# Kernel optimization log

Measured on AMD Instinct MI355X. Metric: run time of the kernel, lower is better.

The kernel has to match this reference:

```python
import math
import jax, jax.numpy as jnp
import numpy as np

LOG_NORM = -0.5 * math.log(2.0 * math.pi)  # per-dim gaussian normalizer
HEADS = 4
EM_ITERS = 5


def _mab(x, wq, bq, wk, bk, wv, bv, wo, bo):
    # Set-Transformer SAB(x) = MAB(x, x), ln=False
    B, S, D = x.shape
    dh = D // HEADS
    q = (x @ wq + bq).reshape(B, S, HEADS, dh)
    k = (x @ wk + bk).reshape(B, S, HEADS, dh)
    v = (x @ wv + bv).reshape(B, S, HEADS, dh)
    att = jax.nn.softmax(jnp.einsum('bqhd,bkhd->bhqk', q, k) / math.sqrt(D), axis=-1)
    o = q + jnp.einsum('bhqk,bkhd->bqhd', att, v)
    o = o.reshape(B, S, D)
    return o + jax.nn.relu(o @ wo + bo)


def setup_inputs() -> dict:
    key = jax.random.key(0)
    ks = jax.random.split(key, 16)
    B, S, D, L, K, MC = 16, 256, 512, 64, 20, 10
    s512 = 1.0 / math.sqrt(512.0)
    inp = {
        'H': jax.random.normal(ks[0], (B, S, D), jnp.float32),
        'eps': jax.random.normal(ks[1], (B * S, MC, L), jnp.float32),
        'sab_wq': jax.random.normal(ks[2], (2, D, D), jnp.float32) * s512,
        'sab_bq': jnp.zeros((2, D), jnp.float32),
        'sab_wk': jax.random.normal(ks[3], (2, D, D), jnp.float32) * s512,
        'sab_bk': jnp.zeros((2, D), jnp.float32),
        'sab_wv': jax.random.normal(ks[4], (2, D, D), jnp.float32) * s512,
        'sab_bv': jnp.zeros((2, D), jnp.float32),
        'sab_wo': jax.random.normal(ks[5], (2, D, D), jnp.float32) * s512,
        'sab_bo': jnp.zeros((2, D), jnp.float32),
        'wz': jax.random.normal(ks[6], (D, 2 * L), jnp.float32) * 0.02,
        'bz': jnp.zeros((2 * L,), jnp.float32),
        'w1': jax.random.normal(ks[7], (L, 2 * D), jnp.float32) * (1.0 / math.sqrt(L)),
        'b1': jnp.zeros((2 * D,), jnp.float32),
        'w2': jax.random.normal(ks[8], (2 * D, 2 * D), jnp.float32) * (1.0 / math.sqrt(2 * D)),
        'b2': jnp.zeros((2 * D,), jnp.float32),
        'w3': jax.random.normal(ks[9], (2 * D, D), jnp.float32) * (1.0 / math.sqrt(2 * D)),
        'b3': jnp.zeros((D,), jnp.float32),
    }
    rng = np.random.default_rng(1)
    # component_size distinct indices into the S*MC latent samples, per batch
    inp['init_idx'] = jnp.asarray(
        np.stack([rng.permutation(S * MC)[:K] for _ in range(B)]).astype(np.int32))
    return inp


def reference(H, eps, init_idx, sab_wq, sab_bq, sab_wk, sab_bk, sab_wv, sab_bv,
              sab_wo, sab_bo, wz, bz, w1, b1, w2, b2, w3, b3):
    B, S, D = H.shape
    MC, L = eps.shape[1], eps.shape[2]
    K = init_idx.shape[1]

    # q(z|x): two SABs + linear head
    h = H
    for i in range(2):
        h = _mab(h, sab_wq[i], sab_bq[i], sab_wk[i], sab_bk[i],
                 sab_wv[i], sab_bv[i], sab_wo[i], sab_bo[i])
    stats = h @ wz + bz                                    # [B,S,2L]
    mean, logvar = stats[..., :L], stats[..., L:]
    std = jnp.exp(0.5 * logvar)
    z = mean.reshape(B * S, 1, L) + eps * std.reshape(B * S, 1, L)
    z = z.reshape(B, S, MC, L)
    all_z = z.reshape(B, S * MC, L)                        # [B,N,L]

    # unsupervised EM prior (unit-variance GMM); distances via expansion
    pi = jnp.full((B, K), 1.0 / K, dtype=H.dtype)
    mu = jnp.take_along_axis(all_z, init_idx[:, :, None], axis=1)  # [B,K,L]
    x2 = jnp.sum(all_z * all_z, axis=-1)                   # [B,N]
    for _ in range(EM_ITERS):
        m2 = jnp.sum(mu * mu, axis=-1)                     # [B,K]
        ll = (-0.5 * (x2[:, :, None] - 2.0 * jnp.einsum('bnd,bkd->bnk', all_z, mu)
                      + m2[:, None, :]) + L * LOG_NORM + jnp.log(pi)[:, None, :])
        post = jax.nn.softmax(ll, axis=-1)                 # [B,N,K]
        Nk = post.sum(axis=1)                              # [B,K]
        pi = Nk / Nk.sum(axis=-1, keepdims=True)
        mu = jnp.einsum('bnk,bnd->bkd', post, all_z) / Nk[:, :, None]
    pi = jax.lax.stop_gradient(pi)
    mu = jax.lax.stop_gradient(mu)

    # reconstruction
    zf = z.reshape(-1, L)
    hr = jax.nn.relu(zf @ w1 + b1)
    hr = jax.nn.relu(hr @ w2 + b2)
    hr = jax.nn.relu(hr @ w3 + b3)
    hr = hr.reshape(B, S, MC, D)
    rec_loss = jnp.sum((hr - H[:, :, None, :]) ** 2) / (B * S * MC)

    # KL
    log_qz = jnp.sum(-0.5 * (logvar[:, :, None, :]
                             + (z - mean[:, :, None, :]) ** 2 / jnp.exp(logvar)[:, :, None, :])
                     + LOG_NORM, axis=-1)                  # [B,S,MC]
    z2 = jnp.sum(z * z, axis=-1)                           # [B,S,MC]
    m2 = jnp.sum(mu * mu, axis=-1)                         # [B,K]
    ll = (-0.5 * (z2[..., None] - 2.0 * jnp.einsum('bsmd,bkd->bsmk', z, mu)
                  + m2[:, None, None, :]) + L * LOG_NORM + jnp.log(pi)[:, None, None, :])
    log_pz = jax.scipy.special.logsumexp(ll, axis=-1)      # [B,S,MC]
    kl_loss = jnp.mean(log_qz - log_pz)
    return rec_loss, kl_loss
```

## Files before the change

### kernel.cpp

```cpp
#include <hip/hip_runtime.h>
#include <hip/hip_bf16.h>
#include <math.h>


#define BATCH 16
#define SEQ 256
#define DIM 512
#define NH 4
#define DH 128
#define LD 64
#define KC 20
#define MC 10
#define NPTS 2560
#define BS_TOT 4096
#define NROWS 40960
#define LOG_NORM (-0.9189385332046727f)

typedef __attribute__((ext_vector_type(8))) short bf16x8;
typedef __attribute__((ext_vector_type(4))) float f32x4;
typedef __hip_bfloat16 bf;

__device__ inline float warpReduceSum(float v) {
    for (int o = 32; o > 0; o >>= 1) v += __shfl_down(v, o);
    return v;
}
__device__ inline float warpReduceMax(float v) {
    for (int o = 32; o > 0; o >>= 1) v = fmaxf(v, __shfl_down(v, o));
    return v;
}

__device__ inline void async_copy16(const bf* g, bf* l) {
    __builtin_amdgcn_global_load_lds(
        (const __attribute__((address_space(1))) unsigned int*)g,
        (__attribute__((address_space(3))) unsigned int*)l, 16, 0, 0);
}

__device__ inline void split_store(float x, bf* ph, bf* pl, long idx) {
    const bf h = __float2bfloat16(x);
    ph[idx] = h;
    pl[idx] = __float2bfloat16(x - __bfloat162float(h));
}

template<int MODE>
__global__ __launch_bounds__(256, 3)
void gemm3t(const bf* __restrict__ Ah, const bf* __restrict__ Al,
            const bf* __restrict__ Bh, const bf* __restrict__ Bl,
            int K, int lda, int ldb,
            const float* __restrict__ b0, const float* __restrict__ b1v,
            const float* __restrict__ b2v,
            float* __restrict__ outF,
            bf* __restrict__ P1h, bf* __restrict__ P1l,
            bf* __restrict__ P2h, bf* __restrict__ P2l,
            bf* __restrict__ P3h, bf* __restrict__ P3l,
            const bf* __restrict__ Rh, const bf* __restrict__ Rl)
{
    __shared__ __align__(16) char smem[24576];
    bf* Ash = (bf*)smem;
    bf* Asl = (bf*)(smem + 4096);
    bf* Bsh = (bf*)(smem + 8192);
    bf* Bsl = (bf*)(smem + 16384);
    float* Xs = (float*)smem;

    const int t = threadIdx.x;
    const int m0 = blockIdx.y * 64, n0 = blockIdx.x * 128;
    const int w = t >> 6, lane = t & 63;
    const int wn = w * 32;
    const int fm = lane & 15, quad = lane >> 4, fk = quad * 8;
    const int srow = t >> 2, scol = (t & 3) * 8;

    f32x4 acc[4][2];
#pragma unroll
    for (int i = 0; i < 4; i++)
#pragma unroll
        for (int j = 0; j < 2; j++) acc[i][j] = (f32x4){0.f, 0.f, 0.f, 0.f};

    const int nk = K >> 5;
    for (int kk = 0; kk < nk; kk++) {
        const long ao = (long)(m0 + srow) * lda + kk * 32 + scol;
        const long bo = (long)(n0 + srow) * ldb + kk * 32 + scol;
        async_copy16(Ah + ao, Ash + w * 512);
        async_copy16(Al + ao, Asl + w * 512);
        async_copy16(Bh + bo, Bsh + w * 512);
        async_copy16(Bh + bo + 64L * ldb, Bsh + 2048 + w * 512);
        async_copy16(Bl + bo, Bsl + w * 512);
        async_copy16(Bl + bo + 64L * ldb, Bsl + 2048 + w * 512);
        __syncthreads();

        bf16x8 afh[4], afl[4], bfh[2], bfl[2];
#pragma unroll
        for (int mi = 0; mi < 4; mi++) {
            afh[mi] = *(const bf16x8*)&Ash[(mi * 16 + fm) * 32 + fk];
            afl[mi] = *(const bf16x8*)&Asl[(mi * 16 + fm) * 32 + fk];
        }
#pragma unroll
        for (int ni = 0; ni < 2; ni++) {
            bfh[ni] = *(const bf16x8*)&Bsh[(wn + ni * 16 + fm) * 32 + fk];
            bfl[ni] = *(const bf16x8*)&Bsl[(wn + ni * 16 + fm) * 32 + fk];
        }
#pragma unroll
        for (int mi = 0; mi < 4; mi++)
#pragma unroll
            for (int ni = 0; ni < 2; ni++) {
                acc[mi][ni] = __builtin_amdgcn_mfma_f32_16x16x32_bf16(
                    afh[mi], bfh[ni], acc[mi][ni], 0, 0, 0);
                acc[mi][ni] = __builtin_amdgcn_mfma_f32_16x16x32_bf16(
                    afh[mi], bfl[ni], acc[mi][ni], 0, 0, 0);
                acc[mi][ni] = __builtin_amdgcn_mfma_f32_16x16x32_bf16(
                    afl[mi], bfh[ni], acc[mi][ni], 0, 0, 0);
            }
        __syncthreads();
    }

    const int rl = t >> 2;
    const int cc4 = (t & 3) * 16;

    for (int p = 0; p < 2; p++) {
        if ((w >> 1) == p) {
            const int cb = wn - p * 64;
#pragma unroll
            for (int mi = 0; mi < 4; mi++)
#pragma unroll
                for (int ni = 0; ni < 2; ni++) {
                    const int c = cb + ni * 16 + fm;
#pragma unroll
                    for (int r = 0; r < 4; r++)
                        Xs[(mi * 16 + quad * 4 + r) * 68 + c] = acc[mi][ni][r];
                }
        }
        __syncthreads();

        if (MODE == 0 && n0 >= 1024) {
            const int hh = (n0 >> 7) & 3;
            const int dd = p * 64 + rl;
            const int bb = m0 >> 8;
            const int sb = (m0 & 255) + cc4;
            const float bias = b2v[hh * 128 + dd];
            const long ob = (((long)(bb * NH + hh) * DH + dd) << 8) + sb;
#pragma unroll
            for (int j = 0; j < 2; j++) {
                bf16x8 vh, vl;
#pragma unroll
                for (int i = 0; i < 8; i++) {
                    const float x = Xs[(cc4 + j * 8 + i) * 68 + rl] + bias;
                    const bf h = __float2bfloat16(x);
                    vh[i] = *(const short*)&h;
                    const bf l = __float2bfloat16(x - __bfloat162float(h));
                    vl[i] = *(const short*)&l;
                }
                *(bf16x8*)&P3h[ob + j * 8] = vh;
                *(bf16x8*)&P3l[ob + j * 8] = vl;
            }
        } else {
            float xv[16];
#pragma unroll
            for (int i = 0; i < 4; i++)
                *(float4*)&xv[i * 4] = *(const float4*)&Xs[rl * 68 + cc4 + i * 4];

            if (MODE == 0) {
                const int which = n0 >> 9;
                const int colq = (n0 & 511) + p * 64 + cc4;
                const float* bias = which ? b1v : b0;
                bf* Ph = which ? P2h : P1h;
                bf* Pl = which ? P2l : P1l;
                const long ob = (long)(m0 + rl) * 512 + colq;
#pragma unroll
                for (int j = 0; j < 2; j++) {
                    bf16x8 vh, vl;
#pragma unroll
                    for (int i = 0; i < 8; i++) {
                        const float x = xv[j * 8 + i] + bias[colq + j * 8 + i];
                        const bf h = __float2bfloat16(x); vh[i] = *(const short*)&h;
                        const bf l = __float2bfloat16(x - __bfloat162float(h));
                        vl[i] = *(const short*)&l;
                    }
                    *(bf16x8*)&Ph[ob + j * 8] = vh;
                    *(bf16x8*)&Pl[ob + j * 8] = vl;
                }
            } else if (MODE == 3) {
                const int colg = n0 + p * 64 + cc4;
                const long ob = (long)(m0 + rl) * 512 + colg;
#pragma unroll
                for (int j = 0; j < 2; j++) {
                    const bf16x8 rh = *(const bf16x8*)&Rh[ob + j * 8];
                    const bf16x8 rv = *(const bf16x8*)&Rl[ob + j * 8];
                    bf16x8 vh, vl;
#pragma unroll
                    for (int i = 0; i < 8; i++) {
                        short sh = rh[i], sl = rv[i];
                        float x = fmaxf(xv[j * 8 + i] + b0[colg + j * 8 + i], 0.f)
                                + __bfloat162float(*(const bf*)&sh)
                                + __bfloat162float(*(const bf*)&sl);
                        const bf h = __float2bfloat16(x); vh[i] = *(const short*)&h;
                        const bf l = __float2bfloat16(x - __bfloat162float(h));
                        vl[i] = *(const short*)&l;
                    }
                    *(bf16x8*)&P1h[ob + j * 8] = vh;
                    *(bf16x8*)&P1l[ob + j * 8] = vl;
                }
            } else {
                const int colg = p * 64 + cc4;
                const long ob = (long)(m0 + rl) * 128 + colg;
#pragma unroll
                for (int i = 0; i < 4; i++) {
                    float4 v = *(float4*)&xv[i * 4];
                    v.x += b0[colg + i * 4 + 0];
                    v.y += b0[colg + i * 4 + 1];
                    v.z += b0[colg + i * 4 + 2];
                    v.w += b0[colg + i * 4 + 3];
                    *(float4*)&outF[ob + i * 4] = v;
                }
            }
        }
        __syncthreads();
    }
}

__global__ __launch_bounds__(256)
void attn_fused(const bf* __restrict__ qh, const bf* __restrict__ ql,
                const bf* __restrict__ kh, const bf* __restrict__ kl,
                const bf* __restrict__ vTh, const bf* __restrict__ vTl,
                bf* __restrict__ oh, bf* __restrict__ ol)
{
    __shared__ __align__(16) char smem[43008];
    bf* Qsh = (bf*)smem;            bf* Qsl = (bf*)(smem + 4096);
    bf* Ksh = (bf*)(smem + 8192);   bf* Ksl = (bf*)(smem + 24576);
    bf* Psh = (bf*)smem;            bf* Psl = (bf*)(smem + 4096);
    bf* Vsh = (bf*)(smem + 8192);   bf* Vsl = (bf*)(smem + 16384);
    float (*red)[4]  = (float(*)[4])(smem + 40960);
    float (*red2)[4] = (float(*)[4])(smem + 41984);

    const int t = threadIdx.x;
    const int z = blockIdx.y;
    const int m0 = blockIdx.x * 64;
    const int bb = z >> 2, hh = z & 3;
    const long hOff = (long)bb * 131072 + (long)hh * 128;
    const long vOff = (long)z * 32768;

    const int w = t >> 6, lane = t & 63;
    const int fm = lane & 15;
    const int quad = lane >> 4;
    const int fk = quad * 8;
    const int srow = t >> 2, scol = (t & 3) * 8;

    f32x4 acc[4][4];
#pragma unroll
    for (int i = 0; i < 4; i++)
#pragma unroll
        for (int j = 0; j < 4; j++) acc[i][j] = (f32x4){0.f, 0.f, 0.f, 0.f};

    for (int kk = 0; kk < 4; kk++) {
        const long ao = hOff + (long)(m0 + srow) * 512 + kk * 32 + scol;
        const long bo = hOff + (long)srow * 512 + kk * 32 + scol;
        async_copy16(qh + ao, Qsh + w * 512);
        async_copy16(ql + ao, Qsl + w * 512);
#pragma unroll
        for (int j = 0; j < 4; j++) {
            async_copy16(kh + bo + (long)j * 64 * 512, Ksh + w * 512 + j * 2048);
            async_copy16(kl + bo + (long)j * 64 * 512, Ksl + w * 512 + j * 2048);
        }
        __syncthreads();

        bf16x8 afh[4], afl[4];
#pragma unroll
        for (int mi = 0; mi < 4; mi++) {
            afh[mi] = *(const bf16x8*)&Qsh[(mi * 16 + fm) * 32 + fk];
            afl[mi] = *(const bf16x8*)&Qsl[(mi * 16 + fm) * 32 + fk];
        }
#pragma unroll
        for (int ni = 0; ni < 4; ni++) {
            const bf16x8 bh = *(const bf16x8*)&Ksh[(w * 64 + ni * 16 + fm) * 32 + fk];
            const bf16x8 bl = *(const bf16x8*)&Ksl[(w * 64 + ni * 16 + fm) * 32 + fk];
#pragma unroll
            for (int mi = 0; mi < 4; mi++) {
                acc[mi][ni] = __builtin_amdgcn_mfma_f32_16x16x32_bf16(
                    afh[mi], bh, acc[mi][ni], 0, 0, 0);
                acc[mi][ni] = __builtin_amdgcn_mfma_f32_16x16x32_bf16(
                    afh[mi], bl, acc[mi][ni], 0, 0, 0);
                acc[mi][ni] = __builtin_amdgcn_mfma_f32_16x16x32_bf16(
                    afl[mi], bh, acc[mi][ni], 0, 0, 0);
            }
        }
        __syncthreads();
    }

    const float alpha = 0.044194173824159216f;
#pragma unroll
    for (int mi = 0; mi < 4; mi++)
#pragma unroll
        for (int r = 0; r < 4; r++) {
            float m = -1e30f;
#pragma unroll
            for (int ni = 0; ni < 4; ni++) m = fmaxf(m, acc[mi][ni][r]);
            for (int o = 8; o > 0; o >>= 1) m = fmaxf(m, __shfl_xor(m, o));
            if (fm == 0) red[mi * 16 + quad * 4 + r][w] = m;
        }
    __syncthreads();
    float invr[4][4];
#pragma unroll
    for (int mi = 0; mi < 4; mi++)
#pragma unroll
        for (int r = 0; r < 4; r++) {
            const int rowl = mi * 16 + quad * 4 + r;
            const float mx = fmaxf(fmaxf(red[rowl][0], red[rowl][1]),
                                   fmaxf(red[rowl][2], red[rowl][3]));
            float s = 0.f;
#pragma unroll
            for (int ni = 0; ni < 4; ni++) {
                const float e = __expf((acc[mi][ni][r] - mx) * alpha);
                acc[mi][ni][r] = e;
                s += e;
            }
            for (int o = 8; o > 0; o >>= 1) s += __shfl_xor(s, o);
            if (fm == 0) red2[rowl][w] = s;
        }
    __syncthreads();
#pragma unroll
    for (int mi = 0; mi < 4; mi++)
#pragma unroll
        for (int r = 0; r < 4; r++) {
            const int rowl = mi * 16 + quad * 4 + r;
            invr[mi][r] = 1.f / (red2[rowl][0] + red2[rowl][1] + red2[rowl][2] + red2[rowl][3]);
        }

    f32x4 acc2[4][2];
#pragma unroll
    for (int i = 0; i < 4; i++)
#pragma unroll
        for (int j = 0; j < 2; j++) acc2[i][j] = (f32x4){0.f, 0.f, 0.f, 0.f};

    for (int kc = 0; kc < 8; kc++) {
        if (w == (kc >> 1)) {
            const int nib = (kc & 1) * 2;
#pragma unroll
            for (int mi = 0; mi < 4; mi++)
#pragma unroll
                for (int r = 0; r < 4; r++) {
                    const int row = mi * 16 + quad * 4 + r;
#pragma unroll
                    for (int j = 0; j < 2; j++) {
                        const float p = acc[mi][nib + j][r] * invr[mi][r];
                        const int cc = j * 16 + fm;
                        const bf h = __float2bfloat16(p);
                        Psh[row * 32 + cc] = h;
                        Psl[row * 32 + cc] = __float2bfloat16(p - __bfloat162float(h));
                    }
                }
        }
        const long vo = vOff + (long)srow * 256 + kc * 32 + scol;
        async_copy16(vTh + vo, Vsh + w * 512);
        async_copy16(vTh + vo + 64L * 256, Vsh + w * 512 + 2048);
        async_copy16(vTl + vo, Vsl + w * 512);
        async_copy16(vTl + vo + 64L * 256, Vsl + w * 512 + 2048);
        __syncthreads();

        bf16x8 pfh[4], pfl[4];
#pragma unroll
        for (int mi = 0; mi < 4; mi++) {
            pfh[mi] = *(const bf16x8*)&Psh[(mi * 16 + fm) * 32 + fk];
            pfl[mi] = *(const bf16x8*)&Psl[(mi * 16 + fm) * 32 + fk];
        }
#pragma unroll
        for (int ni = 0; ni < 2; ni++) {
            const bf16x8 vh = *(const bf16x8*)&Vsh[(w * 32 + ni * 16 + fm) * 32 + fk];
            const bf16x8 vl = *(const bf16x8*)&Vsl[(w * 32 + ni * 16 + fm) * 32 + fk];
#pragma unroll
            for (int mi = 0; mi < 4; mi++) {
                acc2[mi][ni] = __builtin_amdgcn_mfma_f32_16x16x32_bf16(
                    pfh[mi], vh, acc2[mi][ni], 0, 0, 0);
                acc2[mi][ni] = __builtin_amdgcn_mfma_f32_16x16x32_bf16(
                    pfh[mi], vl, acc2[mi][ni], 0, 0, 0);
                acc2[mi][ni] = __builtin_amdgcn_mfma_f32_16x16x32_bf16(
                    pfl[mi], vh, acc2[mi][ni], 0, 0, 0);
            }
        }
        __syncthreads();
    }

#pragma unroll
    for (int ni = 0; ni < 2; ni++) {
        const int col = hh * 128 + w * 32 + ni * 16 + fm;
#pragma unroll
        for (int mi = 0; mi < 4; mi++)
#pragma unroll
            for (int r = 0; r < 4; r++) {
                const int row = mi * 16 + quad * 4 + r;
                const long idx = (long)(bb * 256 + m0 + row) * 512 + col;
                const float x = acc2[mi][ni][r]
                    + __bfloat162float(qh[idx]) + __bfloat162float(ql[idx]);
                split_store(x, oh, ol, idx);
            }
    }
}

template<bool SQLOSS>
__global__ __launch_bounds__(256, 3)
void gemm_mfma(const bf* __restrict__ A, const bf* __restrict__ BT,
               bf* __restrict__ C,
               const float* __restrict__ bias,
               const float* __restrict__ Href,
               float* __restrict__ lossAcc,
               int K, int N)
{
    __shared__ __align__(16) char smem[17408];
    bf* Asg = (bf*)smem;
    bf* Bsg = (bf*)(smem + 8192);
    bf* Cs  = (bf*)smem;
    __shared__ float redS[4];

    const int t = threadIdx.x;
    const int flat = blockIdx.y * gridDim.x + blockIdx.x;
    const int lane8 = flat & 7;
    const int grp = flat >> 3;
    const int n_blk = grp % gridDim.x;
    const int m_blk = (grp / gridDim.x) * 8 + lane8;
    const int m0 = m_blk * 128, n0 = n_blk * 128;

    const int w = t >> 6, lane = t & 63;
    const int wm = (w >> 1) * 64, wn = (w & 1) * 64;
    const int fm = lane & 15;
    const int quad = lane >> 4;
    const int fk = quad * 8;
    const int srow = t >> 2, scol = (t & 3) * 8;

    f32x4 acc[4][4];
#pragma unroll
    for (int i = 0; i < 4; i++)
#pragma unroll
        for (int j = 0; j < 4; j++) acc[i][j] = (f32x4){0.f, 0.f, 0.f, 0.f};

    const int nk = K >> 5;
    for (int kt = 0; kt < nk; kt++) {
        const bf* ga = A + (long)(m0 + srow) * K + kt * 32 + scol;
        const bf* gb = BT + (long)(n0 + srow) * K + kt * 32 + scol;
        async_copy16(ga, Asg + w * 512);
        async_copy16(ga + 64L * K, Asg + 2048 + w * 512);
        async_copy16(gb, Bsg + w * 512);
        async_copy16(gb + 64L * K, Bsg + 2048 + w * 512);
        __syncthreads();

        bf16x8 af[4], bfr[4];
#pragma unroll
        for (int mi = 0; mi < 4; mi++)
            af[mi] = *(const bf16x8*)&Asg[(wm + mi * 16 + fm) * 32 + fk];
#pragma unroll
        for (int ni = 0; ni < 4; ni++)
            bfr[ni] = *(const bf16x8*)&Bsg[(wn + ni * 16 + fm) * 32 + fk];
#pragma unroll
        for (int mi = 0; mi < 4; mi++)
#pragma unroll
            for (int ni = 0; ni < 4; ni++)
                acc[mi][ni] = __builtin_amdgcn_mfma_f32_16x16x32_bf16(
                    af[mi], bfr[ni], acc[mi][ni], 0, 0, 0);
        __syncthreads();
    }

    if (SQLOSS) {
        float lsum = 0.f;
#pragma unroll
        for (int ni = 0; ni < 4; ni++) {
            const int col = n0 + wn + ni * 16 + fm;
            const float b = bias[col];
#pragma unroll
            for (int mi = 0; mi < 4; mi++)
#pragma unroll
                for (int r = 0; r < 4; r++) {
                    const int row = m0 + wm + mi * 16 + quad * 4 + r;
                    const float x = fmaxf(acc[mi][ni][r] + b, 0.f);
                    const float d = x - Href[(long)(row / MC) * DIM + col];
                    lsum = fmaf(d, d, lsum);
                }
        }
        lsum = warpReduceSum(lsum);
        if (lane == 0) redS[w] = lsum;
        __syncthreads();
        if (t == 0) atomicAdd(lossAcc, redS[0] + redS[1] + redS[2] + redS[3]);
    } else {
        for (int hf = 0; hf < 2; hf++) {
            if ((w >> 1) == hf) {
#pragma unroll
                for (int ni = 0; ni < 4; ni++) {
                    const int c = wn + ni * 16 + fm;
                    const float bv = bias[n0 + c];
#pragma unroll
                    for (int mi = 0; mi < 4; mi++)
#pragma unroll
                        for (int r = 0; r < 4; r++) {
                            const float x = fmaxf(acc[mi][ni][r] + bv, 0.f);
                            Cs[(mi * 16 + quad * 4 + r) * 136 + c] = __float2bfloat16(x);
                        }
                }
            }
            __syncthreads();
            const int rl2 = t >> 2, cc2 = (t & 3) * 32;
            const long ob = (long)(m0 + hf * 64 + rl2) * N + n0 + cc2;
#pragma unroll
            for (int j = 0; j < 4; j++)
                *(bf16x8*)&C[ob + j * 8] = *(const bf16x8*)&Cs[rl2 * 136 + cc2 + j * 8];
            __syncthreads();
        }
    }
}

__global__ void conv_all_weights(
    const float* __restrict__ wq, const float* __restrict__ wk,
    const float* __restrict__ wv, const float* __restrict__ wo,
    bf* __restrict__ qkvTh0, bf* __restrict__ qkvTl0,
    bf* __restrict__ woTh0, bf* __restrict__ woTl0,
    bf* __restrict__ qkvTh1, bf* __restrict__ qkvTl1,
    bf* __restrict__ woTh1, bf* __restrict__ woTl1,
    const float* __restrict__ wz, bf* __restrict__ wzTh, bf* __restrict__ wzTl,
    const float* __restrict__ w1, bf* __restrict__ w1T,
    const float* __restrict__ w2, bf* __restrict__ w2T,
    const float* __restrict__ w3, bf* __restrict__ w3T)
{
    const int idx = blockIdx.x * 256 + threadIdx.x;
    if (idx < 2097152) {
        const int layer = idx >> 20;
        const int seg = (idx >> 18) & 3;
        const int r = idx & 262143;
        const int k = r >> 9, n = r & 511;
        const float* src = ((seg == 0) ? wq : (seg == 1) ? wk : (seg == 2) ? wv : wo)
                           + (long)layer * 262144;
        const float x = src[r];
        const bf h = __float2bfloat16(x);
        const bf l = __float2bfloat16(x - __bfloat162float(h));
        if (seg < 3) {
            const long o = (long)(seg * 512 + n) * 512 + k;
            if (layer == 0) { qkvTh0[o] = h; qkvTl0[o] = l; }
            else            { qkvTh1[o] = h; qkvTl1[o] = l; }
        } else {
            const long o = (long)n * 512 + k;
            if (layer == 0) { woTh0[o] = h; woTl0[o] = l; }
            else            { woTh1[o] = h; woTl1[o] = l; }
        }
    } else if (idx < 2162688) {
        const int i = idx - 2097152;
        const int k = i >> 7, n = i & 127;
        const float x = wz[i];
        const bf h = __float2bfloat16(x);
        wzTh[(long)n * 512 + k] = h;
        wzTl[(long)n * 512 + k] = __float2bfloat16(x - __bfloat162float(h));
    } else if (idx < 2228224) {
        const int i = idx - 2162688;
        const int k = i >> 10, n = i & 1023;
        w1T[(long)n * 64 + k] = __float2bfloat16(w1[i]);
    } else if (idx < 3276800) {
        const int i = idx - 2228224;
        const int k = i >> 10, n = i & 1023;
        w2T[(long)n * 1024 + k] = __float2bfloat16(w2[i]);
    } else if (idx < 3801088) {
        const int i = idx - 3276800;
        const int k = i >> 9, n = i & 511;
        w3T[(long)n * 1024 + k] = __float2bfloat16(w3[i]);
    }
}

__global__ void conv_split_flat(const float* __restrict__ src,
                                bf* __restrict__ dh, bf* __restrict__ dl, int n)
{
    const int i = blockIdx.x * 256 + threadIdx.x;
    if (i < n) {
        const float x = src[i];
        const bf h = __float2bfloat16(x);
        dh[i] = h;
        dl[i] = __float2bfloat16(x - __bfloat162float(h));
    }
}

__global__ __launch_bounds__(256)
void zgen(const float* __restrict__ stats, const float* __restrict__ eps,
          float* __restrict__ z, bf* __restrict__ z16)
{
    const int idx = blockIdx.x * 256 + threadIdx.x;
    const int bs = idx / 160;
    const int r = idx % 160;
    const int l4 = r % 16;
    const float4 e = ((const float4*)eps)[idx];
    const float4 mn = ((const float4*)stats)[bs * 32 + l4];
    const float4 lv = ((const float4*)stats)[bs * 32 + 16 + l4];
    float4 zz;
    zz.x = fmaf(e.x, expf(0.5f * lv.x), mn.x);
    zz.y = fmaf(e.y, expf(0.5f * lv.y), mn.y);
    zz.z = fmaf(e.z, expf(0.5f * lv.z), mn.z);
    zz.w = fmaf(e.w, expf(0.5f * lv.w), mn.w);
    ((float4*)z)[idx] = zz;
    bf* zp = z16 + (long)idx * 4;
    zp[0] = __float2bfloat16(zz.x);
    zp[1] = __float2bfloat16(zz.y);
    zp[2] = __float2bfloat16(zz.z);
    zp[3] = __float2bfloat16(zz.w);
}

__global__ void em_init(const float* __restrict__ z, const int* __restrict__ init_idx,
                        float* __restrict__ mu, float* __restrict__ logPi,
                        float* __restrict__ musum, float* __restrict__ NkG)
{
    const int b = blockIdx.x, t = threadIdx.x;
    for (int i = t; i < KC * LD; i += 256) {
        const int k = i >> 6, l = i & 63;
        const int idx = init_idx[b * KC + k];
        mu[b * KC * LD + i] = z[((long)b * NPTS + idx) * LD + l];
        musum[b * KC * LD + i] = 0.f;
    }
    if (t < KC) {
        logPi[b * KC + t] = -logf((float)KC);
        NkG[b * KC + t] = 0.f;
    }
}

__global__ __launch_bounds__(256)
void em_step(const float* __restrict__ z, const float* __restrict__ mu,
             const float* __restrict__ logPi,
             float* __restrict__ musum, float* __restrict__ NkG)
{
    __shared__ float muS[KC][65];
    __shared__ float m2lp[KC];
    __shared__ float postS[KC][256];
    __shared__ float NkS[KC];

    const int tile = blockIdx.x, b = blockIdx.y, t = threadIdx.x;

    for (int i = t; i < KC * LD; i += 256) muS[i >> 6][i & 63] = mu[b * KC * LD + i];
    __syncthreads();
    if (t < KC) {
        float s = 0.f;
        for (int l = 0; l < LD; l++) { const float m = muS[t][l]; s = fmaf(m, m, s); }
        m2lp[t] = -0.5f * s + logPi[b * KC + t];
    }
    __syncthreads();

    const long n = (long)tile * 256 + t;
    const float* zr = &z[((long)b * NPTS + n) * LD];
    float acc[KC];
#pragma unroll
    for (int k = 0; k < KC; k++) acc[k] = 0.f;
#pragma unroll
    for (int l4 = 0; l4 < 16; l4++) {
        const float4 zv = ((const float4*)zr)[l4];
#pragma unroll
        for (int k = 0; k < KC; k++) {
            acc[k] = fmaf(zv.x, muS[k][l4 * 4 + 0], acc[k]);
            acc[k] = fmaf(zv.y, muS[k][l4 * 4 + 1], acc[k]);
            acc[k] = fmaf(zv.z, muS[k][l4 * 4 + 2], acc[k]);
            acc[k] = fmaf(zv.w, muS[k][l4 * 4 + 3], acc[k]);
        }
    }
    float mx = -1e30f;
    float llv[KC];
#pragma unroll
    for (int k = 0; k < KC; k++) { llv[k] = acc[k] + m2lp[k]; mx = fmaxf(mx, llv[k]); }
    float s = 0.f;
#pragma unroll
    for (int k = 0; k < KC; k++) { llv[k] = expf(llv[k] - mx); s += llv[k]; }
    const float inv = 1.f / s;
#pragma unroll
    for (int k = 0; k < KC; k++) postS[k][t] = llv[k] * inv;
    __syncthreads();

    const int lane = t & 63, w = t >> 6;
#pragma unroll
    for (int kk = 0; kk < 5; kk++) {
        const int k = w * 5 + kk;
        float p = postS[k][lane] + postS[k][lane + 64] + postS[k][lane + 128] + postS[k][lane + 192];
        p = warpReduceSum(p);
        if (lane == 0) NkS[k] = p;
    }
    __syncthreads();

    const float* zb = &z[((long)b * NPTS + (long)tile * 256) * LD];
#pragma unroll
    for (int j = 0; j < 5; j++) {
        const int o = t + j * 256;
        const int k = o >> 6, l = o & 63;
        float sacc = 0.f;
        for (int n2 = 0; n2 < 256; n2++)
            sacc = fmaf(postS[k][n2], zb[n2 * LD + l], sacc);
        atomicAdd(&musum[b * KC * LD + o], sacc);
    }
    if (t < KC) atomicAdd(&NkG[b * KC + t], NkS[t]);
}

__global__ void em_update(float* __restrict__ mu, float* __restrict__ logPi,
                          float* __restrict__ musum, float* __restrict__ NkG)
{
    __shared__ float Nk[KC];
    const int b = blockIdx.x, t = threadIdx.x;
    if (t < KC) Nk[t] = NkG[b * KC + t];
    __syncthreads();
    float s = 0.f;
    for (int k = 0; k < KC; k++) s += Nk[k];
    if (t < KC) logPi[b * KC + t] = logf(Nk[t] / s);
    for (int i = t; i < KC * LD; i += 64) {
        const int k = i >> 6;
        mu[b * KC * LD + i] = musum[b * KC * LD + i] / Nk[k];
        musum[b * KC * LD + i] = 0.f;
    }
    __syncthreads();
    if (t < KC) NkG[b * KC + t] = 0.f;
}

__global__ __launch_bounds__(256)
void kl_kernel(const float* __restrict__ z, const float* __restrict__ stats,
               const float* __restrict__ eps,
               const float* __restrict__ mu, const float* __restrict__ logPi,
               float* __restrict__ klAcc)
{
    __shared__ float muS[KC][65];
    __shared__ float m2lp[KC];
    __shared__ float redS[4];

    const int tile = blockIdx.x, b = blockIdx.y, t = threadIdx.x;

    for (int i = t; i < KC * LD; i += 256) muS[i >> 6][i & 63] = mu[b * KC * LD + i];
    __syncthreads();
    if (t < KC) {
        float s = 0.f;
        for (int l = 0; l < LD; l++) { const float m = muS[t][l]; s = fmaf(m, m, s); }
        m2lp[t] = -0.5f * s + logPi[b * KC + t];
    }
    __syncthreads();

    const int n = tile * 256 + t;
    const int sidx = n / MC, m = n % MC;
    const long bs = (long)b * SEQ + sidx;
    const float* zr = &z[((long)b * NPTS + n) * LD];

    float acc[KC];
#pragma unroll
    for (int k = 0; k < KC; k++) acc[k] = 0.f;
    float x2 = 0.f;
#pragma unroll
    for (int l4 = 0; l4 < 16; l4++) {
        const float4 zv = ((const float4*)zr)[l4];
        x2 = fmaf(zv.x, zv.x, fmaf(zv.y, zv.y, fmaf(zv.z, zv.z, fmaf(zv.w, zv.w, x2))));
#pragma unroll
        for (int k = 0; k < KC; k++) {
            acc[k] = fmaf(zv.x, muS[k][l4 * 4 + 0], acc[k]);
            acc[k] = fmaf(zv.y, muS[k][l4 * 4 + 1], acc[k]);
            acc[k] = fmaf(zv.z, muS[k][l4 * 4 + 2], acc[k]);
            acc[k] = fmaf(zv.w, muS[k][l4 * 4 + 3], acc[k]);
        }
    }
    float mx = -1e30f;
    float llv[KC];
#pragma unroll
    for (int k = 0; k < KC; k++) { llv[k] = acc[k] + m2lp[k]; mx = fmaxf(mx, llv[k]); }
    float s = 0.f;
#pragma unroll
    for (int k = 0; k < KC; k++) s += expf(llv[k] - mx);
    const float log_pz = -0.5f * x2 + mx + logf(s) + LD * LOG_NORM;

    const float* lvr = &stats[bs * 128 + 64];
    const float* er = &eps[(bs * MC + m) * LD];
    float slv = 0.f, se2 = 0.f;
#pragma unroll
    for (int l4 = 0; l4 < 16; l4++) {
        const float4 lv = ((const float4*)lvr)[l4];
        slv += lv.x + lv.y + lv.z + lv.w;
        const float4 e = ((const float4*)er)[l4];
        se2 = fmaf(e.x, e.x, fmaf(e.y, e.y, fmaf(e.z, e.z, fmaf(e.w, e.w, se2))));
    }
    const float log_qz = -0.5f * (slv + se2) + LD * LOG_NORM;

    float v = log_qz - log_pz;
    v = warpReduceSum(v);
    if ((t & 63) == 0) redS[t >> 6] = v;
    __syncthreads();
    if (t == 0) atomicAdd(klAcc, redS[0] + redS[1] + redS[2] + redS[3]);
}

__global__ void finalize(const float* __restrict__ scal, float* __restrict__ out)
{
    if (threadIdx.x == 0) {
        out[0] = scal[0] * (1.f / (float)NROWS);
        out[1] = scal[1] * (1.f / (float)NROWS);
    }
}

extern "C" void kernel_launch(void* const* d_in, const int* in_sizes, int n_in,
                              void* d_out, int out_size, void* d_ws, size_t ws_size,
                              hipStream_t stream)
{
    const float* H   = (const float*)d_in[0];
    const float* eps = (const float*)d_in[1];
    const float* wq  = (const float*)d_in[2];
    const float* bq  = (const float*)d_in[3];
    const float* wk  = (const float*)d_in[4];
    const float* bk  = (const float*)d_in[5];
    const float* wv  = (const float*)d_in[6];
    const float* bv  = (const float*)d_in[7];
    const float* wo  = (const float*)d_in[8];
    const float* bo  = (const float*)d_in[9];
    const float* wz  = (const float*)d_in[10];
    const float* bz  = (const float*)d_in[11];
    const float* w1  = (const float*)d_in[12];
    const float* b1  = (const float*)d_in[13];
    const float* w2  = (const float*)d_in[14];
    const float* b2  = (const float*)d_in[15];
    const float* w3  = (const float*)d_in[16];
    const float* b3  = (const float*)d_in[17];
    const int* init_idx = (const int*)d_in[18];
    float* out = (float*)d_out;
    float* wsf = (float*)d_ws;

    const long o_scal  = 0;
    const long o_NkG   = 1024;
    const long o_musum = 2048;
    const long o_logpi = 23552;
    const long o_mu    = 24576;
    const long o_q     = 45056;
    const long o_k     = 2142208;
    const long o_vT    = 4239360;
    const long o_o     = 6336512;
    const long o_h1    = 8433664;
    const long o_qkvT0 = 10530816;
    const long o_woT0  = 11317248;
    const long o_qkvT1 = 11579392;
    const long o_woT1  = 12365824;
    const long o_wzT   = 12627968;
    const long o_st    = 12693504;
    const long o_zb    = 13217792;
    const long o_z16   = 15839232;
    const long o_w1T   = 17149952;
    const long o_w2T   = 17182720;
    const long o_w3T   = 17707008;
    const long o_d1    = 17969152;
    const long o_d2    = 38940672;

    const long PL = (long)BS_TOT * DIM;
    bf* qh  = (bf*)(wsf + o_q);   bf* ql  = qh + PL;
    bf* kh  = (bf*)(wsf + o_k);   bf* kl_ = kh + PL;
    bf* vTh = (bf*)(wsf + o_vT);  bf* vTl = vTh + PL;
    bf* oh  = (bf*)(wsf + o_o);   bf* ol  = oh + PL;
    bf* h1h = (bf*)(wsf + o_h1);  bf* h1l = h1h + PL;
    bf* h2h = qh;                 bf* h2l = ql;
    bf* qkvTh0 = (bf*)(wsf + o_qkvT0); bf* qkvTl0 = qkvTh0 + 1536L * 512;
    bf* woTh0  = (bf*)(wsf + o_woT0);  bf* woTl0  = woTh0 + 512L * 512;
    bf* qkvTh1 = (bf*)(wsf + o_qkvT1); bf* qkvTl1 = qkvTh1 + 1536L * 512;
    bf* woTh1  = (bf*)(wsf + o_woT1);  bf* woTl1  = woTh1 + 512L * 512;
    bf* wzTh = (bf*)(wsf + o_wzT);     bf* wzTl = wzTh + 128L * 512;
    bf* w1T = (bf*)(wsf + o_w1T);
    bf* w2T = (bf*)(wsf + o_w2T);
    bf* w3T = (bf*)(wsf + o_w3T);
    bf* z16 = (bf*)(wsf + o_z16);
    bf* d1  = (bf*)(wsf + o_d1);
    bf* d2  = (bf*)(wsf + o_d2);
    float* st = wsf + o_st;
    float* zb = wsf + o_zb;
    float* scal = wsf + o_scal;

    hipMemsetAsync(scal, 0, 64, stream);

    const dim3 blk(256);

    conv_split_flat<<<(int)((PL + 255) / 256), blk, 0, stream>>>(H, h1h, h1l, (int)PL);
    conv_all_weights<<<14848, blk, 0, stream>>>(
        wq, wk, wv, wo,
        qkvTh0, qkvTl0, woTh0, woTl0,
        qkvTh1, qkvTl1, woTh1, woTl1,
        wz, wzTh, wzTl, w1, w1T, w2, w2T, w3, w3T);

    for (int i = 0; i < 2; i++) {
        const long boff = (long)i * DIM;
        bf* qkh = i ? qkvTh1 : qkvTh0;  bf* qkl = i ? qkvTl1 : qkvTl0;
        bf* wh  = i ? woTh1 : woTh0;    bf* wl  = i ? woTl1 : woTl0;

        gemm3t<0><<<dim3(12, 64), blk, 0, stream>>>(
            h1h, h1l, qkh, qkl, 512, 512, 512,
            bq + boff, bk + boff, bv + boff, nullptr,
            qh, ql, kh, kl_, vTh, vTl, nullptr, nullptr);
        attn_fused<<<dim3(4, 64), blk, 0, stream>>>(qh, ql, kh, kl_, vTh, vTl, oh, ol);
        bf* houth = (i == 0) ? h1h : h2h;
        bf* houtl = (i == 0) ? h1l : h2l;
        gemm3t<3><<<dim3(4, 64), blk, 0, stream>>>(
            oh, ol, wh, wl, 512, 512, 512,
            bo + boff, nullptr, nullptr, nullptr,
            houth, houtl, nullptr, nullptr, nullptr, nullptr, oh, ol);
    }

    gemm3t<4><<<dim3(1, 64), blk, 0, stream>>>(
        h2h, h2l, wzTh, wzTl, 512, 512, 512,
        bz, nullptr, nullptr, st,
        nullptr, nullptr, nullptr, nullptr, nullptr, nullptr, nullptr, nullptr);

    zgen<<<2560, blk, 0, stream>>>(st, eps, zb, z16);

    gemm_mfma<false><<<dim3(8, 320), blk, 0, stream>>>(
        z16, w1T, d1, b1, nullptr, nullptr, 64, 1024);
    gemm_mfma<false><<<dim3(8, 320), blk, 0, stream>>>(
        d1, w2T, d2, b2, nullptr, nullptr, 1024, 1024);
    gemm_mfma<true><<<dim3(4, 320), blk, 0, stream>>>(
        d2, w3T, nullptr, b3, H, scal + 0, 1024, 512);

    em_init<<<16, blk, 0, stream>>>(zb, init_idx, wsf + o_mu, wsf + o_logpi,
                                    wsf + o_musum, wsf + o_NkG);
    for (int it = 0; it < 5; it++) {
        em_step<<<dim3(10, 16), blk, 0, stream>>>(zb, wsf + o_mu, wsf + o_logpi,
                                                  wsf + o_musum, wsf + o_NkG);
        em_update<<<16, 64, 0, stream>>>(wsf + o_mu, wsf + o_logpi,
                                         wsf + o_musum, wsf + o_NkG);
    }

    kl_kernel<<<dim3(10, 16), blk, 0, stream>>>(zb, st, eps, wsf + o_mu,
                                                wsf + o_logpi, scal + 1);

    finalize<<<1, 64, 0, stream>>>(scal, out);
}
```

Baseline: 713.8 us.

## Fuse z generation, EM loop and KL into one cooperative kernel

Replaces zgen, em_init, five em_step/em_update pairs and kl_kernel with a single cooperative kernel of 160 blocks that uses grid-wide syncs between phases. The H split conversion and the scalar zeroing move into the weight-conversion kernel, which removes the memset and one launch. This targets per-launch overhead and gaps across about 13 small dependent launches. In exchange it adds grid.sync costs, relies on all 160 blocks being co-resident, and zgen now runs on only 160 blocks instead of 2560.

Result: slower. 1.453 ms (+103.6%).

```diff
diff --git a/kernel.cpp b/kernel.cpp
--- a/kernel.cpp
+++ b/kernel.cpp
@@ -1,6 +1,9 @@
 #include <hip/hip_runtime.h>
 #include <hip/hip_bf16.h>
+#include <hip/hip_cooperative_groups.h>
 #include <math.h>
+
+namespace cg = cooperative_groups;
 
 
 #define BATCH 16
@@ -22,10 +25,6 @@
 
 __device__ inline float warpReduceSum(float v) {
     for (int o = 32; o > 0; o >>= 1) v += __shfl_down(v, o);
-    return v;
-}
-__device__ inline float warpReduceMax(float v) {
-    for (int o = 32; o > 0; o >>= 1) v = fmaxf(v, __shfl_down(v, o));
     return v;
 }
 
@@ -501,7 +500,8 @@
     }
 }
 
-__global__ void conv_all_weights(
+__global__ void conv_all(
+    const float* __restrict__ H, bf* __restrict__ h0h, bf* __restrict__ h0l,
     const float* __restrict__ wq, const float* __restrict__ wk,
     const float* __restrict__ wv, const float* __restrict__ wo,
     bf* __restrict__ qkvTh0, bf* __restrict__ qkvTl0,
@@ -511,9 +511,20 @@
     const float* __restrict__ wz, bf* __restrict__ wzTh, bf* __restrict__ wzTl,
     const float* __restrict__ w1, bf* __restrict__ w1T,
     const float* __restrict__ w2, bf* __restrict__ w2T,
-    const float* __restrict__ w3, bf* __restrict__ w3T)
+    const float* __restrict__ w3, bf* __restrict__ w3T,
+    float* __restrict__ scal)
 {
-    const int idx = blockIdx.x * 256 + threadIdx.x;
+    const int t = threadIdx.x;
+    if (blockIdx.x == 0 && t < 16) scal[t] = 0.f;
+    const int gidx = blockIdx.x * 256 + t;
+    if (gidx < 2097152) {
+        const float x = H[gidx];
+        const bf h = __float2bfloat16(x);
+        h0h[gidx] = h;
+        h0l[gidx] = __float2bfloat16(x - __bfloat162float(h));
+        return;
+    }
+    const int idx = gidx - 2097152;
     if (idx < 2097152) {
         const int layer = idx >> 20;
         const int seg = (idx >> 18) & 3;
@@ -555,70 +566,138 @@
     }
 }
 
-__global__ void conv_split_flat(const float* __restrict__ src,
-                                bf* __restrict__ dh, bf* __restrict__ dl, int n)
-{
-    const int i = blockIdx.x * 256 + threadIdx.x;
-    if (i < n) {
-        const float x = src[i];
-        const bf h = __float2bfloat16(x);
-        dh[i] = h;
-        dl[i] = __float2bfloat16(x - __bfloat162float(h));
-    }
-}
-
 __global__ __launch_bounds__(256)
-void zgen(const float* __restrict__ stats, const float* __restrict__ eps,
-          float* __restrict__ z, bf* __restrict__ z16)
-{
-    const int idx = blockIdx.x * 256 + threadIdx.x;
-    const int bs = idx / 160;
-    const int r = idx % 160;
-    const int l4 = r % 16;
-    const float4 e = ((const float4*)eps)[idx];
-    const float4 mn = ((const float4*)stats)[bs * 32 + l4];
-    const float4 lv = ((const float4*)stats)[bs * 32 + 16 + l4];
-    float4 zz;
-    zz.x = fmaf(e.x, expf(0.5f * lv.x), mn.x);
-    zz.y = fmaf(e.y, expf(0.5f * lv.y), mn.y);
-    zz.z = fmaf(e.z, expf(0.5f * lv.z), mn.z);
-    zz.w = fmaf(e.w, expf(0.5f * lv.w), mn.w);
-    ((float4*)z)[idx] = zz;
-    bf* zp = z16 + (long)idx * 4;
-    zp[0] = __float2bfloat16(zz.x);
-    zp[1] = __float2bfloat16(zz.y);
-    zp[2] = __float2bfloat16(zz.z);
-    zp[3] = __float2bfloat16(zz.w);
-}
-
-__global__ void em_init(const float* __restrict__ z, const int* __restrict__ init_idx,
-                        float* __restrict__ mu, float* __restrict__ logPi,
-                        float* __restrict__ musum, float* __restrict__ NkG)
-{
-    const int b = blockIdx.x, t = threadIdx.x;
-    for (int i = t; i < KC * LD; i += 256) {
-        const int k = i >> 6, l = i & 63;
-        const int idx = init_idx[b * KC + k];
-        mu[b * KC * LD + i] = z[((long)b * NPTS + idx) * LD + l];
-        musum[b * KC * LD + i] = 0.f;
-    }
-    if (t < KC) {
-        logPi[b * KC + t] = -logf((float)KC);
-        NkG[b * KC + t] = 0.f;
-    }
-}
-
-__global__ __launch_bounds__(256)
-void em_step(const float* __restrict__ z, const float* __restrict__ mu,
-             const float* __restrict__ logPi,
-             float* __restrict__ musum, float* __restrict__ NkG)
+void em_all(const float* __restrict__ stats, const float* __restrict__ eps,
+            const int* __restrict__ init_idx,
+            float* __restrict__ z, bf* __restrict__ z16,
+            float* __restrict__ mu, float* __restrict__ logPi,
+            float* __restrict__ musum, float* __restrict__ NkG,
+            float* __restrict__ klAcc)
 {
     __shared__ float muS[KC][65];
     __shared__ float m2lp[KC];
     __shared__ float postS[KC][256];
     __shared__ float NkS[KC];
-
-    const int tile = blockIdx.x, b = blockIdx.y, t = threadIdx.x;
+    __shared__ float NkU[KC];
+    __shared__ float redS[4];
+
+    cg::grid_group grid = cg::this_grid();
+    const int bx = blockIdx.x;
+    const int tile = bx % 10, b = bx / 10;
+    const int t = threadIdx.x;
+    const int lane = t & 63, w = t >> 6;
+
+    for (int i = 0; i < 16; i++) {
+        const int idx = bx * 4096 + i * 256 + t;
+        const int bs = idx / 160;
+        const int r = idx % 160;
+        const int l4 = r % 16;
+        const float4 e = ((const float4*)eps)[idx];
+        const float4 mn = ((const float4*)stats)[bs * 32 + l4];
+        const float4 lv = ((const float4*)stats)[bs * 32 + 16 + l4];
+        float4 zz;
+        zz.x = fmaf(e.x, expf(0.5f * lv.x), mn.x);
+        zz.y = fmaf(e.y, expf(0.5f * lv.y), mn.y);
+        zz.z = fmaf(e.z, expf(0.5f * lv.z), mn.z);
+        zz.w = fmaf(e.w, expf(0.5f * lv.w), mn.w);
+        ((float4*)z)[idx] = zz;
+        bf* zp = z16 + (long)idx * 4;
+        zp[0] = __float2bfloat16(zz.x);
+        zp[1] = __float2bfloat16(zz.y);
+        zp[2] = __float2bfloat16(zz.z);
+        zp[3] = __float2bfloat16(zz.w);
+    }
+    grid.sync();
+
+    if (tile == 0) {
+        for (int i = t; i < KC * LD; i += 256) {
+            const int k = i >> 6, l = i & 63;
+            const int idx = init_idx[b * KC + k];
+            mu[b * KC * LD + i] = z[((long)b * NPTS + idx) * LD + l];
+            musum[b * KC * LD + i] = 0.f;
+        }
+        if (t < KC) {
+            logPi[b * KC + t] = -logf((float)KC);
+            NkG[b * KC + t] = 0.f;
+        }
+    }
+    grid.sync();
+
+    for (int it = 0; it < 5; it++) {
+        for (int i = t; i < KC * LD; i += 256) muS[i >> 6][i & 63] = mu[b * KC * LD + i];
+        __syncthreads();
+        if (t < KC) {
+            float s = 0.f;
+            for (int l = 0; l < LD; l++) { const float m = muS[t][l]; s = fmaf(m, m, s); }
+            m2lp[t] = -0.5f * s + logPi[b * KC + t];
+        }
+        __syncthreads();
+
+        const long n = (long)tile * 256 + t;
+        const float* zr = &z[((long)b * NPTS + n) * LD];
+        float acc[KC];
+#pragma unroll
+        for (int k = 0; k < KC; k++) acc[k] = 0.f;
+#pragma unroll
+        for (int l4 = 0; l4 < 16; l4++) {
+            const float4 zv = ((const float4*)zr)[l4];
+#pragma unroll
+            for (int k = 0; k < KC; k++) {
+                acc[k] = fmaf(zv.x, muS[k][l4 * 4 + 0], acc[k]);
+                acc[k] = fmaf(zv.y, muS[k][l4 * 4 + 1], acc[k]);
+                acc[k] = fmaf(zv.z, muS[k][l4 * 4 + 2], acc[k]);
+                acc[k] = fmaf(zv.w, muS[k][l4 * 4 + 3], acc[k]);
+            }
+        }
+        float mx = -1e30f;
+        float llv[KC];
+#pragma unroll
+        for (int k = 0; k < KC; k++) { llv[k] = acc[k] + m2lp[k]; mx = fmaxf(mx, llv[k]); }
+        float s = 0.f;
+#pragma unroll
+        for (int k = 0; k < KC; k++) { llv[k] = expf(llv[k] - mx); s += llv[k]; }
+        const float inv = 1.f / s;
+#pragma unroll
+        for (int k = 0; k < KC; k++) postS[k][t] = llv[k] * inv;
+        __syncthreads();
+
+#pragma unroll
+        for (int kk = 0; kk < 5; kk++) {
+            const int k = w * 5 + kk;
+            float p = postS[k][lane] + postS[k][lane + 64] + postS[k][lane + 128] + postS[k][lane + 192];
+            p = warpReduceSum(p);
+            if (lane == 0) NkS[k] = p;
+        }
+        __syncthreads();
+
+        const float* zb = &z[((long)b * NPTS + (long)tile * 256) * LD];
+#pragma unroll
+        for (int j = 0; j < 5; j++) {
+            const int o = t + j * 256;
+            const int k = o >> 6, l = o & 63;
+            float sacc = 0.f;
+            for (int n2 = 0; n2 < 256; n2++)
+                sacc = fmaf(postS[k][n2], zb[n2 * LD + l], sacc);
+            atomicAdd(&musum[b * KC * LD + o], sacc);
+        }
+        if (t < KC) atomicAdd(&NkG[b * KC + t], NkS[t]);
+        grid.sync();
+
+        if (tile == 0) {
+            if (t < KC) NkU[t] = NkG[b * KC + t];
+            __syncthreads();
+            float sn = 0.f;
+            for (int k = 0; k < KC; k++) sn += NkU[k];
+            if (t < KC) logPi[b * KC + t] = logf(NkU[t] / sn);
+            for (int i = t; i < KC * LD; i += 256) {
+                mu[b * KC * LD + i] = musum[b * KC * LD + i] / NkU[i >> 6];
+                musum[b * KC * LD + i] = 0.f;
+            }
+            __syncthreads();
+            if (t < KC) NkG[b * KC + t] = 0.f;
+        }
+        grid.sync();
+    }
 
     for (int i = t; i < KC * LD; i += 256) muS[i >> 6][i & 63] = mu[b * KC * LD + i];
     __syncthreads();
@@ -629,144 +708,55 @@
     }
     __syncthreads();
 
-    const long n = (long)tile * 256 + t;
-    const float* zr = &z[((long)b * NPTS + n) * LD];
-    float acc[KC];
-#pragma unroll
-    for (int k = 0; k < KC; k++) acc[k] = 0.f;
-#pragma unroll
-    for (int l4 = 0; l4 < 16; l4++) {
-        const float4 zv = ((const float4*)zr)[l4];
-#pragma unroll
-        for (int k = 0; k < KC; k++) {
-            acc[k] = fmaf(zv.x, muS[k][l4 * 4 + 0], acc[k]);
-            acc[k] = fmaf(zv.y, muS[k][l4 * 4 + 1], acc[k]);
-            acc[k] = fmaf(zv.z, muS[k][l4 * 4 + 2], acc[k]);
-            acc[k] = fmaf(zv.w, muS[k][l4 * 4 + 3], acc[k]);
-        }
-    }
-    float mx = -1e30f;
-    float llv[KC];
-#pragma unroll
-    for (int k = 0; k < KC; k++) { llv[k] = acc[k] + m2lp[k]; mx = fmaxf(mx, llv[k]); }
-    float s = 0.f;
-#pragma unroll
-    for (int k = 0; k < KC; k++) { llv[k] = expf(llv[k] - mx); s += llv[k]; }
-    const float inv = 1.f / s;
-#pragma unroll
-    for (int k = 0; k < KC; k++) postS[k][t] = llv[k] * inv;
-    __syncthreads();
-
-    const int lane = t & 63, w = t >> 6;
-#pragma unroll
-    for (int kk = 0; kk < 5; kk++) {
-        const int k = w * 5 + kk;
-        float p = postS[k][lane] + postS[k][lane + 64] + postS[k][lane + 128] + postS[k][lane + 192];
-        p = warpReduceSum(p);
-        if (lane == 0) NkS[k] = p;
-    }
-    __syncthreads();
-
-    const float* zb = &z[((long)b * NPTS + (long)tile * 256) * LD];
-#pragma unroll
-    for (int j = 0; j < 5; j++) {
-        const int o = t + j * 256;
-        const int k = o >> 6, l = o & 63;
-        float sacc = 0.f;
-        for (int n2 = 0; n2 < 256; n2++)
-            sacc = fmaf(postS[k][n2], zb[n2 * LD + l], sacc);
-        atomicAdd(&musum[b * KC * LD + o], sacc);
-    }
-    if (t < KC) atomicAdd(&NkG[b * KC + t], NkS[t]);
-}
-
-__global__ void em_update(float* __restrict__ mu, float* __restrict__ logPi,
-                          float* __restrict__ musum, float* __restrict__ NkG)
-{
-    __shared__ float Nk[KC];
-    const int b = blockIdx.x, t = threadIdx.x;
-    if (t < KC) Nk[t] = NkG[b * KC + t];
-    __syncthreads();
-    float s = 0.f;
-    for (int k = 0; k < KC; k++) s += Nk[k];
-    if (t < KC) logPi[b * KC + t] = logf(Nk[t] / s);
-    for (int i = t; i < KC * LD; i += 64) {
-        const int k = i >> 6;
-        mu[b * KC * LD + i] = musum[b * KC * LD + i] / Nk[k];
-        musum[b * KC * LD + i] = 0.f;
-    }
-    __syncthreads();
-    if (t < KC) NkG[b * KC + t] = 0.f;
-}
-
-__global__ __launch_bounds__(256)
-void kl_kernel(const float* __restrict__ z, const float* __restrict__ stats,
-               const float* __restrict__ eps,
-               const float* __restrict__ mu, const float* __restrict__ logPi,
-               float* __restrict__ klAcc)
-{
-    __shared__ float muS[KC][65];
-    __shared__ float m2lp[KC];
-    __shared__ float redS[4];
-
-    const int tile = blockIdx.x, b = blockIdx.y, t = threadIdx.x;
-
-    for (int i = t; i < KC * LD; i += 256) muS[i >> 6][i & 63] = mu[b * KC * LD + i];
-    __syncthreads();
-    if (t < KC) {
+    {
+        const int n = tile * 256 + t;
+        const int sidx = n / MC, m = n % MC;
+        const long bs = (long)b * SEQ + sidx;
+        const float* zr = &z[((long)b * NPTS + n) * LD];
+
+        float acc[KC];
+#pragma unroll
+        for (int k = 0; k < KC; k++) acc[k] = 0.f;
+        float x2 = 0.f;
+#pragma unroll
+        for (int l4 = 0; l4 < 16; l4++) {
+            const float4 zv = ((const float4*)zr)[l4];
+            x2 = fmaf(zv.x, zv.x, fmaf(zv.y, zv.y, fmaf(zv.z, zv.z, fmaf(zv.w, zv.w, x2))));
+#pragma unroll
+            for (int k = 0; k < KC; k++) {
+                acc[k] = fmaf(zv.x, muS[k][l4 * 4 + 0], acc[k]);
+                acc[k] = fmaf(zv.y, muS[k][l4 * 4 + 1], acc[k]);
+                acc[k] = fmaf(zv.z, muS[k][l4 * 4 + 2], acc[k]);
+                acc[k] = fmaf(zv.w, muS[k][l4 * 4 + 3], acc[k]);
+            }
+        }
+        float mx = -1e30f;
+        float llv[KC];
+#pragma unroll
+        for (int k = 0; k < KC; k++) { llv[k] = acc[k] + m2lp[k]; mx = fmaxf(mx, llv[k]); }
         float s = 0.f;
-        for (int l = 0; l < LD; l++) { const float m = muS[t][l]; s = fmaf(m, m, s); }
-        m2lp[t] = -0.5f * s + logPi[b * KC + t];
-    }
-    __syncthreads();
-
-    const int n = tile * 256 + t;
-    const int sidx = n / MC, m = n % MC;
-    const long bs = (long)b * SEQ + sidx;
-    const float* zr = &z[((long)b * NPTS + n) * LD];
-
-    float acc[KC];
-#pragma unroll
-    for (int k = 0; k < KC; k++) acc[k] = 0.f;
-    float x2 = 0.f;
-#pragma unroll
-    for (int l4 = 0; l4 < 16; l4++) {
-        const float4 zv = ((const float4*)zr)[l4];
-        x2 = fmaf(zv.x, zv.x, fmaf(zv.y, zv.y, fmaf(zv.z, zv.z, fmaf(zv.w, zv.w, x2))));
-#pragma unroll
-        for (int k = 0; k < KC; k++) {
-            acc[k] = fmaf(zv.x, muS[k][l4 * 4 + 0], acc[k]);
-            acc[k] = fmaf(zv.y, muS[k][l4 * 4 + 1], acc[k]);
-            acc[k] = fmaf(zv.z, muS[k][l4 * 4 + 2], acc[k]);
-            acc[k] = fmaf(zv.w, muS[k][l4 * 4 + 3], acc[k]);
-        }
-    }
-    float mx = -1e30f;
-    float llv[KC];
-#pragma unroll
-    for (int k = 0; k < KC; k++) { llv[k] = acc[k] + m2lp[k]; mx = fmaxf(mx, llv[k]); }
-    float s = 0.f;
-#pragma unroll
-    for (int k = 0; k < KC; k++) s += expf(llv[k] - mx);
-    const float log_pz = -0.5f * x2 + mx + logf(s) + LD * LOG_NORM;
-
-    const float* lvr = &stats[bs * 128 + 64];
-    const float* er = &eps[(bs * MC + m) * LD];
-    float slv = 0.f, se2 = 0.f;
-#pragma unroll
-    for (int l4 = 0; l4 < 16; l4++) {
-        const float4 lv = ((const float4*)lvr)[l4];
-        slv += lv.x + lv.y + lv.z + lv.w;
-        const float4 e = ((const float4*)er)[l4];
-        se2 = fmaf(e.x, e.x, fmaf(e.y, e.y, fmaf(e.z, e.z, fmaf(e.w, e.w, se2))));
-    }
-    const float log_qz = -0.5f * (slv + se2) + LD * LOG_NORM;
-
-    float v = log_qz - log_pz;
-    v = warpReduceSum(v);
-    if ((t & 63) == 0) redS[t >> 6] = v;
-    __syncthreads();
-    if (t == 0) atomicAdd(klAcc, redS[0] + redS[1] + redS[2] + redS[3]);
+#pragma unroll
+        for (int k = 0; k < KC; k++) s += expf(llv[k] - mx);
+        const float log_pz = -0.5f * x2 + mx + logf(s) + LD * LOG_NORM;
+
+        const float* lvr = &stats[bs * 128 + 64];
+        const float* er = &eps[(bs * MC + m) * LD];
+        float slv = 0.f, se2 = 0.f;
+#pragma unroll
+        for (int l4 = 0; l4 < 16; l4++) {
+            const float4 lv = ((const float4*)lvr)[l4];
+            slv += lv.x + lv.y + lv.z + lv.w;
+            const float4 e = ((const float4*)er)[l4];
+            se2 = fmaf(e.x, e.x, fmaf(e.y, e.y, fmaf(e.z, e.z, fmaf(e.w, e.w, se2))));
+        }
+        const float log_qz = -0.5f * (slv + se2) + LD * LOG_NORM;
+
+        float v = log_qz - log_pz;
+        v = warpReduceSum(v);
+        if ((t & 63) == 0) redS[t >> 6] = v;
+        __syncthreads();
+        if (t == 0) atomicAdd(klAcc, redS[0] + redS[1] + redS[2] + redS[3]);
+    }
 }
 
 __global__ void finalize(const float* __restrict__ scal, float* __restrict__ out)
@@ -848,17 +838,19 @@
     float* st = wsf + o_st;
     float* zb = wsf + o_zb;
     float* scal = wsf + o_scal;
-
-    hipMemsetAsync(scal, 0, 64, stream);
+    float* muP = wsf + o_mu;
+    float* lpP = wsf + o_logpi;
+    float* msP = wsf + o_musum;
+    float* nkP = wsf + o_NkG;
 
     const dim3 blk(256);
 
-    conv_split_flat<<<(int)((PL + 255) / 256), blk, 0, stream>>>(H, h1h, h1l, (int)PL);
-    conv_all_weights<<<14848, blk, 0, stream>>>(
+    conv_all<<<23040, blk, 0, stream>>>(
+        H, h1h, h1l,
         wq, wk, wv, wo,
         qkvTh0, qkvTl0, woTh0, woTl0,
         qkvTh1, qkvTl1, woTh1, woTl1,
-        wz, wzTh, wzTl, w1, w1T, w2, w2T, w3, w3T);
+        wz, wzTh, wzTl, w1, w1T, w2, w2T, w3, w3T, scal);
 
     for (int i = 0; i < 2; i++) {
         const long boff = (long)i * DIM;
@@ -883,7 +875,18 @@
         bz, nullptr, nullptr, st,
         nullptr, nullptr, nullptr, nullptr, nullptr, nullptr, nullptr, nullptr);
 
-    zgen<<<2560, blk, 0, stream>>>(st, eps, zb, z16);
+    {
+        const float* st_c = st;
+        const float* eps_c = eps;
+        const int* ii_c = init_idx;
+        float* z_p = zb;  bf* z16_p = z16;
+        float* kl_p = scal + 1;
+        void* kargs[] = { (void*)&st_c, (void*)&eps_c, (void*)&ii_c,
+                          (void*)&z_p, (void*)&z16_p,
+                          (void*)&muP, (void*)&lpP, (void*)&msP, (void*)&nkP,
+                          (void*)&kl_p };
+        hipLaunchCooperativeKernel((void*)em_all, dim3(160), blk, kargs, 0, stream);
+    }
 
     gemm_mfma<false><<<dim3(8, 320), blk, 0, stream>>>(
         z16, w1T, d1, b1, nullptr, nullptr, 64, 1024);
@@ -892,17 +895,5 @@
     gemm_mfma<true><<<dim3(4, 320), blk, 0, stream>>>(
         d2, w3T, nullptr, b3, H, scal + 0, 1024, 512);
 
-    em_init<<<16, blk, 0, stream>>>(zb, init_idx, wsf + o_mu, wsf + o_logpi,
-                                    wsf + o_musum, wsf + o_NkG);
-    for (int it = 0; it < 5; it++) {
-        em_step<<<dim3(10, 16), blk, 0, stream>>>(zb, wsf + o_mu, wsf + o_logpi,
-                                                  wsf + o_musum, wsf + o_NkG);
-        em_update<<<16, 64, 0, stream>>>(wsf + o_mu, wsf + o_logpi,
-                                         wsf + o_musum, wsf + o_NkG);
-    }
-
-    kl_kernel<<<dim3(10, 16), blk, 0, stream>>>(zb, st, eps, wsf + o_mu,
-                                                wsf + o_logpi, scal + 1);
-
     finalize<<<1, 64, 0, stream>>>(scal, out);
 }
```
